# Optimization experiments

Measured on AMD Instinct MI355X. Metric: run time of the kernel, lower is better.

## Reference

```python
import jax, jax.numpy as jnp
import numpy as np

B, L, C, D = 8, 8192, 256, 256


def setup_inputs() -> dict:
    key = jax.random.key(0)
    ks = jax.random.split(key, 13)
    bound = 1.0 / np.sqrt(C)

    def W(k):
        return jax.random.uniform(k, (C, D), jnp.float32, -bound, bound)

    def b(k):
        return jax.random.uniform(k, (D,), jnp.float32, -bound, bound)

    return {
        "xs": jax.random.normal(ks[0], (B, L, C), jnp.float32),
        # forward-direction params
        "Wh1": W(ks[1]), "bh1": b(ks[2]),
        "Wz1": W(ks[3]), "bz1": b(ks[4]),
        "Ws1": W(ks[5]), "bs1": b(ks[6]),
        "h01": jnp.zeros((1, 1, D), jnp.float32),
        # backward-direction params
        "Wh_1": W(ks[7]), "bh_1": b(ks[8]),
        "Wz_1": W(ks[9]), "bz_1": b(ks[10]),
        "Ws_1": W(ks[11]), "bs_1": b(ks[12]),
        "h0_1": jnp.zeros((1, 1, D), jnp.float32),
    }


def _gru_scan(z, h_tilde, h0):
    """h[t] = z[t]*h_tilde[t] + (1-z[t])*h[t-1], h[-1]=h0. Parallel over time
    via associative scan on the affine maps h -> a*h + b."""
    a = 1.0 - z            # [B, L, D]
    b = z * h_tilde        # [B, L, D]

    def combine(c1, c2):
        a1, b1 = c1
        a2, b2 = c2
        return a1 * a2, a2 * b1 + b2

    A, Bc = jax.lax.associative_scan(combine, (a, b), axis=1)
    return Bc + A * h0     # broadcast h0 [1,1,D]


def reference(xs, Wh1, bh1, Wz1, bz1, Ws1, bs1, h01,
              Wh_1, bh_1, Wz_1, bz_1, Ws_1, bs_1, h0_1):
    sig = jax.nn.sigmoid
    # forward direction
    hf = _gru_scan(sig(xs @ Wz1 + bz1), xs @ Wh1 + bh1, h01) * sig(xs @ Ws1 + bs1)
    # backward direction: reverse time, scan, reverse back
    zr = sig(xs @ Wz_1 + bz_1)
    hr = xs @ Wh_1 + bh_1
    hb = _gru_scan(zr[:, ::-1], hr[:, ::-1], h0_1)[:, ::-1] * sig(xs @ Ws_1 + bs_1)
    return hf + hb
```

## Files before the change

kernel.cpp:

```cpp
#include <hip/hip_runtime.h>
#include <hip/hip_bf16.h>

typedef unsigned short u16;

#define BDIM 8
#define LDIM 8192
#define KDIM 256
#define DDIM 256
#define MTOT 65536
#define NDIM 1536
#define TCH  32
#define NCH  256


typedef float floatx4 __attribute__((ext_vector_type(4)));
typedef short bf16x8 __attribute__((ext_vector_type(8)));
typedef unsigned int u32x4 __attribute__((ext_vector_type(4)));
typedef unsigned int u32x2 __attribute__((ext_vector_type(2)));
typedef float f32x2 __attribute__((ext_vector_type(2)));

__device__ __forceinline__ u16 f2bf(float f) {
  union { __hip_bfloat16 h; u16 u; } c;
  c.h = __float2bfloat16(f);
  return c.u;
}
__device__ __forceinline__ float bf2f(u16 u) {
  union { unsigned int i; float f; } c;
  c.i = ((unsigned int)u) << 16;
  return c.f;
}
__device__ __forceinline__ float sigmoidf_fast(float x) {
  return __builtin_amdgcn_rcpf(1.0f + __expf(-x));
}
__device__ __forceinline__ void gll16(const u16* g, u16* l) {
  __builtin_amdgcn_global_load_lds((const __attribute__((address_space(1))) void*)g,
                                   (__attribute__((address_space(3))) void*)l, 16, 0, 0);
}

__global__ void prep_conv(const float* __restrict__ Wh1, const float* __restrict__ Wz1,
                          const float* __restrict__ Ws1, const float* __restrict__ Wh_1,
                          const float* __restrict__ Wz_1, const float* __restrict__ Ws_1,
                          const float* __restrict__ bh1, const float* __restrict__ bz1,
                          const float* __restrict__ bs1, const float* __restrict__ bh_1,
                          const float* __restrict__ bz_1, const float* __restrict__ bs_1,
                          u16* __restrict__ WcatT, float* __restrict__ bcat,
                          const float* __restrict__ xs, u16* __restrict__ Abf) {
  if (blockIdx.x < NDIM) {
    const int n = blockIdx.x;
    const int k = threadIdx.x;
    const int nn = n & 63;
    const int p = (n & ~63) | ((nn & 15) << 2) | (nn >> 4);
    const int dir = p / 768, r = p % 768;
    int d; const float* W; const float* bb;
    if (r < 512) {
      d = r >> 1;
      if (r & 1) { W = dir ? Wz_1 : Wz1; bb = dir ? bz_1 : bz1; }
      else       { W = dir ? Wh_1 : Wh1; bb = dir ? bh_1 : bh1; }
    } else {
      d = r - 512;
      W = dir ? Ws_1 : Ws1; bb = dir ? bs_1 : bs1;
    }
    WcatT[(size_t)n * KDIM + k] = f2bf(W[k * DDIM + d]);
    if (k == 0) bcat[p] = bb[d];
  } else {
    const int cb = blockIdx.x - NDIM;
#pragma unroll
    for (int pass = 0; pass < 4; ++pass) {
      size_t i = ((size_t)(pass * 2048 + cb) * 256 + threadIdx.x) * 8;
      const float4* s = (const float4*)(xs + i);
      float4 f0 = s[0], f1 = s[1];
      union { u16 u[8]; u32x4 v; } t;
      t.u[0] = f2bf(f0.x); t.u[1] = f2bf(f0.y); t.u[2] = f2bf(f0.z); t.u[3] = f2bf(f0.w);
      t.u[4] = f2bf(f1.x); t.u[5] = f2bf(f1.y); t.u[6] = f2bf(f1.z); t.u[7] = f2bf(f1.w);
      *(u32x4*)(Abf + i) = t.v;
    }
  }
}

__global__ __launch_bounds__(256) void gemm_kernel(const u16* __restrict__ Abf,
                                                   const u16* __restrict__ WcatT,
                                                   const float* __restrict__ bcat,
                                                   u16* __restrict__ G,
                                                   float* __restrict__ Acc,
                                                   float* __restrict__ Bcc) {
  __shared__ __align__(16) u16 sm[16384];
  u16* As = sm;
  u16* Bs = sm + 8192;
  const int tid = threadIdx.x;
  const int lane = tid & 63, wave = tid >> 6;
  const int wm = wave >> 1, wn = wave & 1;
  const int q = lane >> 4, r = lane & 15;

  const int xcd = blockIdx.x & 7;
  const int li  = blockIdx.x >> 3;
  const int mt  = xcd * 64 + li / 12;
  const int nt  = li % 12;
  const int m0 = mt * 128, n0 = nt * 128;

  const u16* gA[4]; const u16* gB[4]; u16* lA[4]; u16* lB[4];
#pragma unroll
  for (int j = 0; j < 4; j++) {
    const int bi = wave * 256 + j * 64 + lane;
    const int row = bi >> 3;
    const int kq = (bi & 7) ^ (row & 7);
    gA[j] = Abf   + (size_t)(m0 + row) * KDIM + kq * 8;
    gB[j] = WcatT + (size_t)(n0 + row) * KDIM + kq * 8;
    lA[j] = As + bi * 8;
    lB[j] = Bs + bi * 8;
  }

  floatx4 acc[4][4];
  floatx4 z4 = {0.f, 0.f, 0.f, 0.f};
#pragma unroll
  for (int i = 0; i < 4; i++)
#pragma unroll
    for (int j = 0; j < 4; j++) acc[i][j] = z4;

  for (int k0 = 0; k0 < KDIM; k0 += 64) {
#pragma unroll
    for (int j = 0; j < 4; j++) { gll16(gA[j] + k0, lA[j]); gll16(gB[j] + k0, lB[j]); }
    __syncthreads();
#pragma unroll
    for (int kk = 0; kk < 2; kk++) {
      bf16x8 af[4], bv[4];
#pragma unroll
      for (int i = 0; i < 4; i++) {
        const int row = wm * 64 + i * 16 + r;
        af[i] = *(const bf16x8*)(As + (row * 8 + ((kk * 4 + q) ^ (row & 7))) * 8);
      }
#pragma unroll
      for (int j = 0; j < 4; j++) {
        const int row = wn * 64 + j * 16 + r;
        bv[j] = *(const bf16x8*)(Bs + (row * 8 + ((kk * 4 + q) ^ (row & 7))) * 8);
      }
#pragma unroll
      for (int i = 0; i < 4; i++)
#pragma unroll
        for (int j = 0; j < 4; j++)
          acc[i][j] = __builtin_amdgcn_mfma_f32_16x16x32_bf16(af[i], bv[j], acc[i][j], 0, 0, 0);
    }
    __syncthreads();
  }

  const int pcol = wn * 64 + (r << 2);
  const float4 bv4 = *(const float4*)(bcat + n0 + pcol);
  const int hz = (n0 % 768) < 512;

  if (hz) {
#pragma unroll
    for (int i = 0; i < 4; i++) {
#pragma unroll
      for (int reg = 0; reg < 4; reg++) {
        const int lrow = wm * 64 + i * 16 + q * 4 + reg;
        union { u16 u[4]; u32x2 v; } t;
        t.u[0] = f2bf(acc[i][0][reg] + bv4.x);
        t.u[1] = f2bf(acc[i][1][reg] + bv4.y);
        t.u[2] = f2bf(acc[i][2][reg] + bv4.z);
        t.u[3] = f2bf(acc[i][3][reg] + bv4.w);
        *(u32x2*)(sm + lrow * 128 + pcol) = t.v;
      }
    }

    __syncthreads();

#pragma unroll
    for (int p = 0; p < 8; p++) {
      const int idx = p * 2048 + tid * 8;
      const int row = idx >> 7, col = idx & 127;
      const u32x4 v = *(const u32x4*)(sm + idx);
      __builtin_nontemporal_store(v, (u32x4*)(G + (size_t)(m0 + row) * NDIM + n0 + col));
    }

    const int cc = wave;
    const int dd = lane;
    const int dirn = n0 / 768;
    const int dbase = (n0 % 768) >> 1;
    const int bb = m0 >> 13;
    const int c0 = (m0 & 8191) >> 5;
    float h = 0.f, P = 1.f;
#pragma unroll 8
    for (int i = 0; i < TCH; ++i) {
      const int tl = dirn ? (TCH - 1 - i) : i;
      const unsigned int hzv = *(const unsigned int*)(sm + (cc * 32 + tl) * 128 + dd * 2);
      const float z = sigmoidf_fast(bf2f((u16)(hzv >> 16)));
      const float a = 1.f - z;
      h = fmaf(a, h, z * bf2f((u16)(hzv & 0xffffu)));
      P *= a;
    }
    const size_t u = (size_t)dirn * 2048 + (size_t)bb * 256 + (size_t)(c0 + cc);
    Acc[u * 256 + dbase + dd] = P;
    Bcc[u * 256 + dbase + dd] = h;
  } else {
#pragma unroll
    for (int i = 0; i < 4; i++) {
#pragma unroll
      for (int reg = 0; reg < 4; reg++) {
        const int lrow = wm * 64 + i * 16 + q * 4 + reg;
        union { u16 u[4]; u32x2 v; } t;
        t.u[0] = f2bf(acc[i][0][reg] + bv4.x);
        t.u[1] = f2bf(acc[i][1][reg] + bv4.y);
        t.u[2] = f2bf(acc[i][2][reg] + bv4.z);
        t.u[3] = f2bf(acc[i][3][reg] + bv4.w);
        __builtin_nontemporal_store(t.v, (u32x2*)(G + (size_t)(m0 + lrow) * NDIM + n0 + pcol));
      }
    }
  }
}

__global__ void scan_phaseB(const float* __restrict__ Acc, const float* __restrict__ Bcc,
                            const float* __restrict__ h01, const float* __restrict__ h0_1,
                            float* __restrict__ Pref) {
  const int d = threadIdx.x, b = blockIdx.x, dir = blockIdx.y;
  float h = dir ? h0_1[d] : h01[d];
  const size_t ubase = ((size_t)dir * BDIM + b) * NCH;
  if (dir == 0) {
    for (int c0 = 0; c0 < NCH; c0 += 16) {
      float a[16], bb[16];
#pragma unroll
      for (int j = 0; j < 16; ++j) {
        size_t idx = (ubase + c0 + j) * DDIM + d;
        a[j] = Acc[idx]; bb[j] = Bcc[idx];
      }
#pragma unroll
      for (int j = 0; j < 16; ++j) {
        Pref[(ubase + c0 + j) * DDIM + d] = h;
        h = fmaf(a[j], h, bb[j]);
      }
    }
  } else {
    for (int c0 = NCH - 1; c0 >= 0; c0 -= 16) {
      float a[16], bb[16];
#pragma unroll
      for (int j = 0; j < 16; ++j) {
        size_t idx = (ubase + c0 - j) * DDIM + d;
        a[j] = Acc[idx]; bb[j] = Bcc[idx];
      }
#pragma unroll
      for (int j = 0; j < 16; ++j) {
        Pref[(ubase + c0 - j) * DDIM + d] = h;
        h = fmaf(a[j], h, bb[j]);
      }
    }
  }
}

__global__ __launch_bounds__(256) void scan_phaseC(const u16* __restrict__ G,
                                                   const float* __restrict__ Pref,
                                                   float* __restrict__ out) {
  __shared__ float obuf[TCH * 256];
  const int c = blockIdx.x & 255, b = blockIdx.x >> 8;
  const int dir = threadIdx.x >> 7;
  const int ld  = threadIdx.x & 127;
  const int d0 = ld * 2;
  const int u = dir * 2048 + b * 256 + c;
  const float2 h2 = *(const float2*)(Pref + (size_t)u * 256 + d0);
  float h0 = h2.x, h1 = h2.y;
  const u16* ghz = G + (size_t)b * LDIM * NDIM + dir * 768 + d0 * 2;
  const u16* gs  = G + (size_t)b * LDIM * NDIM + dir * 768 + 512 + d0;

#pragma unroll
  for (int i = 0; i < 16; ++i) {
    const int tl = dir ? (TCH - 1 - i) : i;
    const int t = c * TCH + tl;
    const uint2 hz4 = *(const uint2*)(ghz + (size_t)t * NDIM);
    const unsigned int s2 = *(const unsigned int*)(gs + (size_t)t * NDIM);
    const float z0 = sigmoidf_fast(bf2f((u16)(hz4.x >> 16)));
    const float z1 = sigmoidf_fast(bf2f((u16)(hz4.y >> 16)));
    h0 = fmaf(1.f - z0, h0, z0 * bf2f((u16)(hz4.x & 0xffffu)));
    h1 = fmaf(1.f - z1, h1, z1 * bf2f((u16)(hz4.y & 0xffffu)));
    float2 o;
    o.x = h0 * sigmoidf_fast(bf2f((u16)(s2 & 0xffffu)));
    o.y = h1 * sigmoidf_fast(bf2f((u16)(s2 >> 16)));
    *(float2*)(obuf + tl * 256 + d0) = o;
  }

  __syncthreads();

#pragma unroll
  for (int i = 16; i < 32; ++i) {
    const int tl = dir ? (TCH - 1 - i) : i;
    const int t = c * TCH + tl;
    const uint2 hz4 = *(const uint2*)(ghz + (size_t)t * NDIM);
    const unsigned int s2 = *(const unsigned int*)(gs + (size_t)t * NDIM);
    const float z0 = sigmoidf_fast(bf2f((u16)(hz4.x >> 16)));
    const float z1 = sigmoidf_fast(bf2f((u16)(hz4.y >> 16)));
    h0 = fmaf(1.f - z0, h0, z0 * bf2f((u16)(hz4.x & 0xffffu)));
    h1 = fmaf(1.f - z1, h1, z1 * bf2f((u16)(hz4.y & 0xffffu)));
    const float o0 = h0 * sigmoidf_fast(bf2f((u16)(s2 & 0xffffu)));
    const float o1 = h1 * sigmoidf_fast(bf2f((u16)(s2 >> 16)));
    const float2 other = *(const float2*)(obuf + tl * 256 + d0);
    f32x2 res;
    res.x = o0 + other.x;
    res.y = o1 + other.y;
    __builtin_nontemporal_store(res, (f32x2*)(out + ((size_t)b * LDIM + t) * DDIM + d0));
  }
}

extern "C" void kernel_launch(void* const* d_in, const int* in_sizes, int n_in,
                              void* d_out, int out_size, void* d_ws, size_t ws_size,
                              hipStream_t stream) {
  const float* xs   = (const float*)d_in[0];
  const float* Wh1  = (const float*)d_in[1];
  const float* bh1  = (const float*)d_in[2];
  const float* Wz1  = (const float*)d_in[3];
  const float* bz1  = (const float*)d_in[4];
  const float* Ws1  = (const float*)d_in[5];
  const float* bs1  = (const float*)d_in[6];
  const float* h01  = (const float*)d_in[7];
  const float* Wh_1 = (const float*)d_in[8];
  const float* bh_1 = (const float*)d_in[9];
  const float* Wz_1 = (const float*)d_in[10];
  const float* bz_1 = (const float*)d_in[11];
  const float* Ws_1 = (const float*)d_in[12];
  const float* bs_1 = (const float*)d_in[13];
  const float* h0_1 = (const float*)d_in[14];
  float* out = (float*)d_out;

  char* ws = (char*)d_ws;
  u16* WcatT = (u16*)ws;   ws += (size_t)NDIM * KDIM * 2;
  float* bcat = (float*)ws; ws += (size_t)NDIM * 4;
  u16* Abf = (u16*)ws;     ws += (size_t)MTOT * KDIM * 2;
  u16* G = (u16*)ws;       ws += (size_t)MTOT * NDIM * 2;

  const size_t sumElems = (size_t)2 * BDIM * NCH * DDIM;
  float* Acc  = (float*)ws; ws += sumElems * 4;
  float* Bcc  = (float*)ws; ws += sumElems * 4;
  float* Pref = (float*)ws; ws += sumElems * 4;
  if ((size_t)(ws - (char*)d_ws) > ws_size) return;

  prep_conv<<<dim3(NDIM + 2048), dim3(256), 0, stream>>>(
      Wh1, Wz1, Ws1, Wh_1, Wz_1, Ws_1, bh1, bz1, bs1, bh_1, bz_1, bs_1,
      WcatT, bcat, xs, Abf);
  gemm_kernel<<<dim3(6144), dim3(256), 0, stream>>>(Abf, WcatT, bcat, G, Acc, Bcc);
  scan_phaseB<<<dim3(BDIM, 2), dim3(DDIM), 0, stream>>>(Acc, Bcc, h01, h0_1, Pref);
  scan_phaseC<<<dim3(2048), dim3(256), 0, stream>>>(G, Pref, out);
}
```

Baseline: 273.7 us.

## Split chunk-carry scan into two-level hierarchical scan and drop nontemporal stores

```diff
diff --git a/kernel.cpp b/kernel.cpp
--- a/kernel.cpp
+++ b/kernel.cpp
@@ -11,13 +11,13 @@
 #define NDIM 1536
 #define TCH  32
 #define NCH  256
+#define NSUP 16
 
 
 typedef float floatx4 __attribute__((ext_vector_type(4)));
 typedef short bf16x8 __attribute__((ext_vector_type(8)));
 typedef unsigned int u32x4 __attribute__((ext_vector_type(4)));
 typedef unsigned int u32x2 __attribute__((ext_vector_type(2)));
-typedef float f32x2 __attribute__((ext_vector_type(2)));
 
 __device__ __forceinline__ u16 f2bf(float f) {
   union { __hip_bfloat16 h; u16 u; } c;
@@ -168,7 +168,7 @@
       const int idx = p * 2048 + tid * 8;
       const int row = idx >> 7, col = idx & 127;
       const u32x4 v = *(const u32x4*)(sm + idx);
-      __builtin_nontemporal_store(v, (u32x4*)(G + (size_t)(m0 + row) * NDIM + n0 + col));
+      *(u32x4*)(G + (size_t)(m0 + row) * NDIM + n0 + col) = v;
     }
 
     const int cc = wave;
@@ -201,51 +201,64 @@
         t.u[1] = f2bf(acc[i][1][reg] + bv4.y);
         t.u[2] = f2bf(acc[i][2][reg] + bv4.z);
         t.u[3] = f2bf(acc[i][3][reg] + bv4.w);
-        __builtin_nontemporal_store(t.v, (u32x2*)(G + (size_t)(m0 + lrow) * NDIM + n0 + pcol));
+        *(u32x2*)(G + (size_t)(m0 + lrow) * NDIM + n0 + pcol) = t.v;
       }
     }
   }
 }
 
-__global__ void scan_phaseB(const float* __restrict__ Acc, const float* __restrict__ Bcc,
-                            const float* __restrict__ h01, const float* __restrict__ h0_1,
-                            float* __restrict__ Pref) {
+__global__ __launch_bounds__(256) void scan_phaseB1(float* __restrict__ Acc,
+                                                    float* __restrict__ Bcc,
+                                                    float* __restrict__ Asum,
+                                                    float* __restrict__ Bsum) {
+  const int d = threadIdx.x;
+  const int s   = blockIdx.x & 15;
+  const int b   = (blockIdx.x >> 4) & 7;
+  const int dir = blockIdx.x >> 7;
+  const size_t ubase = ((size_t)dir * BDIM + b) * NCH;
+  float a[16], bb[16];
+#pragma unroll
+  for (int i = 0; i < 16; ++i) {
+    const int c = dir ? (NCH - 1 - (s * 16 + i)) : (s * 16 + i);
+    const size_t idx = (ubase + c) * DDIM + d;
+    a[i] = Acc[idx]; bb[i] = Bcc[idx];
+  }
+  float A = 1.f, Bv = 0.f;
+#pragma unroll
+  for (int i = 0; i < 16; ++i) {
+    const int c = dir ? (NCH - 1 - (s * 16 + i)) : (s * 16 + i);
+    const size_t idx = (ubase + c) * DDIM + d;
+    Acc[idx] = A; Bcc[idx] = Bv;
+    Bv = fmaf(a[i], Bv, bb[i]);
+    A  = a[i] * A;
+  }
+  const size_t sidx = (((size_t)dir * BDIM + b) * NSUP + s) * DDIM + d;
+  Asum[sidx] = A; Bsum[sidx] = Bv;
+}
+
+__global__ void scan_phaseB2(const float* __restrict__ Asum, const float* __restrict__ Bsum,
+                             const float* __restrict__ h01, const float* __restrict__ h0_1,
+                             float* __restrict__ Hsup) {
   const int d = threadIdx.x, b = blockIdx.x, dir = blockIdx.y;
   float h = dir ? h0_1[d] : h01[d];
-  const size_t ubase = ((size_t)dir * BDIM + b) * NCH;
-  if (dir == 0) {
-    for (int c0 = 0; c0 < NCH; c0 += 16) {
-      float a[16], bb[16];
-#pragma unroll
-      for (int j = 0; j < 16; ++j) {
-        size_t idx = (ubase + c0 + j) * DDIM + d;
-        a[j] = Acc[idx]; bb[j] = Bcc[idx];
-      }
-#pragma unroll
-      for (int j = 0; j < 16; ++j) {
-        Pref[(ubase + c0 + j) * DDIM + d] = h;
-        h = fmaf(a[j], h, bb[j]);
-      }
-    }
-  } else {
-    for (int c0 = NCH - 1; c0 >= 0; c0 -= 16) {
-      float a[16], bb[16];
-#pragma unroll
-      for (int j = 0; j < 16; ++j) {
-        size_t idx = (ubase + c0 - j) * DDIM + d;
-        a[j] = Acc[idx]; bb[j] = Bcc[idx];
-      }
-#pragma unroll
-      for (int j = 0; j < 16; ++j) {
-        Pref[(ubase + c0 - j) * DDIM + d] = h;
-        h = fmaf(a[j], h, bb[j]);
-      }
-    }
+  const size_t base = ((size_t)dir * BDIM + b) * NSUP;
+  float A[16], Bv[16];
+#pragma unroll
+  for (int s = 0; s < 16; ++s) {
+    A[s]  = Asum[(base + s) * DDIM + d];
+    Bv[s] = Bsum[(base + s) * DDIM + d];
+  }
+#pragma unroll
+  for (int s = 0; s < 16; ++s) {
+    Hsup[(base + s) * DDIM + d] = h;
+    h = fmaf(A[s], h, Bv[s]);
   }
 }
 
 __global__ __launch_bounds__(256) void scan_phaseC(const u16* __restrict__ G,
-                                                   const float* __restrict__ Pref,
+                                                   const float* __restrict__ Acc,
+                                                   const float* __restrict__ Bcc,
+                                                   const float* __restrict__ Hsup,
                                                    float* __restrict__ out) {
   __shared__ float obuf[TCH * 256];
   const int c = blockIdx.x & 255, b = blockIdx.x >> 8;
@@ -253,8 +266,12 @@
   const int ld  = threadIdx.x & 127;
   const int d0 = ld * 2;
   const int u = dir * 2048 + b * 256 + c;
-  const float2 h2 = *(const float2*)(Pref + (size_t)u * 256 + d0);
-  float h0 = h2.x, h1 = h2.y;
+  const int sp = dir ? ((NCH - 1 - c) >> 4) : (c >> 4);
+  const float2 hs = *(const float2*)(Hsup + ((((size_t)dir * BDIM + b) * NSUP + sp) * DDIM) + d0);
+  const float2 ap = *(const float2*)(Acc + (size_t)u * 256 + d0);
+  const float2 bp = *(const float2*)(Bcc + (size_t)u * 256 + d0);
+  float h0 = fmaf(ap.x, hs.x, bp.x);
+  float h1 = fmaf(ap.y, hs.y, bp.y);
   const u16* ghz = G + (size_t)b * LDIM * NDIM + dir * 768 + d0 * 2;
   const u16* gs  = G + (size_t)b * LDIM * NDIM + dir * 768 + 512 + d0;
 
@@ -289,10 +306,10 @@
     const float o0 = h0 * sigmoidf_fast(bf2f((u16)(s2 & 0xffffu)));
     const float o1 = h1 * sigmoidf_fast(bf2f((u16)(s2 >> 16)));
     const float2 other = *(const float2*)(obuf + tl * 256 + d0);
-    f32x2 res;
+    float2 res;
     res.x = o0 + other.x;
     res.y = o1 + other.y;
-    __builtin_nontemporal_store(res, (f32x2*)(out + ((size_t)b * LDIM + t) * DDIM + d0));
+    *(float2*)(out + ((size_t)b * LDIM + t) * DDIM + d0) = res;
   }
 }
 
@@ -323,15 +340,19 @@
   u16* G = (u16*)ws;       ws += (size_t)MTOT * NDIM * 2;
 
   const size_t sumElems = (size_t)2 * BDIM * NCH * DDIM;
+  const size_t supElems = (size_t)2 * BDIM * NSUP * DDIM;
   float* Acc  = (float*)ws; ws += sumElems * 4;
   float* Bcc  = (float*)ws; ws += sumElems * 4;
-  float* Pref = (float*)ws; ws += sumElems * 4;
+  float* Asum = (float*)ws; ws += supElems * 4;
+  float* Bsum = (float*)ws; ws += supElems * 4;
+  float* Hsup = (float*)ws; ws += supElems * 4;
   if ((size_t)(ws - (char*)d_ws) > ws_size) return;
 
   prep_conv<<<dim3(NDIM + 2048), dim3(256), 0, stream>>>(
       Wh1, Wz1, Ws1, Wh_1, Wz_1, Ws_1, bh1, bz1, bs1, bh_1, bz_1, bs_1,
       WcatT, bcat, xs, Abf);
   gemm_kernel<<<dim3(6144), dim3(256), 0, stream>>>(Abf, WcatT, bcat, G, Acc, Bcc);
-  scan_phaseB<<<dim3(BDIM, 2), dim3(DDIM), 0, stream>>>(Acc, Bcc, h01, h0_1, Pref);
-  scan_phaseC<<<dim3(2048), dim3(256), 0, stream>>>(G, Pref, out);
-}
+  scan_phaseB1<<<dim3(256), dim3(DDIM), 0, stream>>>(Acc, Bcc, Asum, Bsum);
+  scan_phaseB2<<<dim3(BDIM, 2), dim3(DDIM), 0, stream>>>(Asum, Bsum, h01, h0_1, Hsup);
+  scan_phaseC<<<dim3(2048), dim3(256), 0, stream>>>(G, Acc, Bcc, Hsup, out);
+}
```

Result: no change. 269.6 us (-1.5%).
